# Kernel optimization log

Measured on AMD Instinct MI355X. Metric: run time of the kernel, lower is better.

Reference implementation:

```python
import jax, jax.numpy as jnp
import numpy as np

B, L, IN_DIM, OUT_DIM = 65536, 9, 128, 64


def setup_inputs() -> dict:
    key = jax.random.key(0)
    ks = jax.random.split(key, 9)
    s1 = 1.0 / np.sqrt(2 * IN_DIM)
    s2 = 1.0 / np.sqrt(IN_DIM)
    return {
        "value": jax.random.normal(ks[0], (B, L, IN_DIM), dtype=jnp.float32),
        "key": jax.random.normal(ks[1], (B, IN_DIM), dtype=jnp.float32),
        "seq_len": jax.random.randint(ks[2], (B,), 0, 8, dtype=jnp.int64),
        "maxlen": 9,
        # get_w: Linear(2*in_dim, in_dim) -> ReLU -> Linear(in_dim, 1)
        "w1": jax.random.uniform(ks[3], (IN_DIM, 2 * IN_DIM), jnp.float32, -s1, s1),
        "b1": jax.random.uniform(ks[4], (IN_DIM,), jnp.float32, -s1, s1),
        "w2": jax.random.uniform(ks[5], (1, IN_DIM), jnp.float32, -s2, s2),
        "b2": jax.random.uniform(ks[6], (1,), jnp.float32, -s2, s2),
        # fc: Linear(in_dim, out_dim) -> ReLU
        "fcw": jax.random.uniform(ks[7], (OUT_DIM, IN_DIM), jnp.float32, -s2, s2),
        "fcb": jax.random.uniform(ks[8], (OUT_DIM,), jnp.float32, -s2, s2),
    }


def reference(value, key, seq_len, maxlen, w1, b1, w2, b2, fcw, fcb):
    # value: [B, L, D]; key: [B, D]; L == maxlen
    Lv = value.shape[1]
    key_rep = jnp.broadcast_to(key[:, None, :], value.shape)          # [B, L, D]
    cat = jnp.concatenate([key_rep, value], axis=-1)                  # [B, L, 2D]
    h = jax.nn.relu(jnp.einsum("bld,hd->blh", cat, w1) + b1)          # [B, L, D]
    weight = (jnp.einsum("blh,oh->blo", h, w2) + b2)[..., 0]          # [B, L]
    # sequence_mask(seq_len + 1, maxlen): position t valid iff t+1 <= seq_len+1
    pos = jnp.arange(1, Lv + 1)                                       # [L]
    mask = pos[None, :] <= (seq_len + 1)[:, None]                     # [B, L] bool
    weight = jnp.where(mask, weight, -jnp.inf)
    attn = jax.nn.softmax(weight, axis=-1)                            # [B, L]
    out = jnp.einsum("bld,bl->bd", value, attn)                       # [B, D]
    out = jax.nn.relu(out @ fcw.T + fcb)                              # [B, out_dim]
    return out
```

## Files before the change

### kernel.cpp

```cpp
#include <hip/hip_runtime.h>
#include <hip/hip_bf16.h>

typedef __attribute__((ext_vector_type(8))) short short8;
typedef __attribute__((ext_vector_type(4))) float f32x4;

#define NW 8
#define BPW 16
#define BPB (NW * BPW)

static __device__ __forceinline__ unsigned pk_bf16(float a, float b) {
    unsigned d;
    asm("v_cvt_pk_bf16_f32 %0, %1, %2" : "=v"(d) : "v"(a), "v"(b));
    return d;
}

static __device__ __forceinline__ unsigned rne16(float x) {
    unsigned u = __float_as_uint(x);
    return (u + 0x7fffu + ((u >> 16) & 1u)) >> 16;
}
static __device__ __forceinline__ unsigned rne_bf16_pair(float x, float y) {
    return rne16(x) | (rne16(y) << 16);
}

static __device__ __forceinline__ short8 pack_frag(f32x4 a, f32x4 b) {
    union { unsigned u[4]; short8 s; } u;
    u.u[0] = pk_bf16(a.x, a.y);
    u.u[1] = pk_bf16(a.z, a.w);
    u.u[2] = pk_bf16(b.x, b.y);
    u.u[3] = pk_bf16(b.z, b.w);
    return u.s;
}

static __device__ __forceinline__ void stage_bfrags(const float* __restrict__ w,
                                                    int row_stride, int k_off, int nct,
                                                    short8* lds, int tid) {
    const int total = 4 * nct * 64;
    for (int idx = tid; idx < total; idx += NW * 64) {
        int lane = idx & 63;
        int ct = (idx >> 6) % nct;
        int kt = idx / (64 * nct);
        int n = ct * 16 + (lane & 15);
        int k = kt * 32 + (lane >> 4) * 8;
        const float* p = w + (size_t)n * row_stride + k_off + k;
        f32x4 a = *(const f32x4*)p;
        f32x4 b = *(const f32x4*)(p + 4);
        lds[idx] = pack_frag(a, b);
    }
}

static __device__ __forceinline__ void stage_bfrags_split(const float* __restrict__ w,
                                                          int row_stride, int nct,
                                                          short8* lds_hi, short8* lds_lo,
                                                          int tid) {
    const int total = 4 * nct * 64;
    for (int idx = tid; idx < total; idx += NW * 64) {
        int lane = idx & 63;
        int ct = (idx >> 6) % nct;
        int kt = idx / (64 * nct);
        int n = ct * 16 + (lane & 15);
        int k = kt * 32 + (lane >> 4) * 8;
        const float* p = w + (size_t)n * row_stride + k;
        f32x4 a = *(const f32x4*)p;
        f32x4 b = *(const f32x4*)(p + 4);
        float xs[8] = {a.x, a.y, a.z, a.w, b.x, b.y, b.z, b.w};
        union { unsigned u[4]; short8 s; } uh, ul;
#pragma unroll
        for (int q = 0; q < 4; ++q) {
            float x = xs[2 * q], y = xs[2 * q + 1];
            unsigned hx = rne16(x), hy = rne16(y);
            uh.u[q] = hx | (hy << 16);
            ul.u[q] = rne_bf16_pair(x - __uint_as_float(hx << 16),
                                    y - __uint_as_float(hy << 16));
        }
        lds_hi[idx] = uh.s;
        lds_lo[idx] = ul.s;
    }
}

__global__ __launch_bounds__(NW * 64, 2)
void mask_attn_fused(const float* __restrict__ value, const float* __restrict__ key,
                     const int* __restrict__ seq_len, const float* __restrict__ w1,
                     const float* __restrict__ b1, const float* __restrict__ w2,
                     const float* __restrict__ fcw, const float* __restrict__ fcb,
                     float* __restrict__ out, int B) {
    __shared__ short8 wlds[2048];

    const int tid = threadIdx.x;
    const int wave = tid >> 6;
    const int lane = tid & 63;
    const int g = lane >> 4;
    const int lo = lane & 15;

    const long long b0w = (long long)blockIdx.x * BPB + (long long)wave * BPW;
    long long vb = b0w + lo; if (vb > (long long)B - 1) vb = (long long)B - 1;

    stage_bfrags(w1, 2 * 128, 0, 8, wlds, tid);
    __syncthreads();

    unsigned hkp[8][2];
    {
        const float* kp = key + vb * 128 + g * 8;
        short8 af[4];
#pragma unroll
        for (int kt = 0; kt < 4; ++kt)
            af[kt] = pack_frag(*(const f32x4*)(kp + kt * 32), *(const f32x4*)(kp + kt * 32 + 4));
#pragma unroll
        for (int ct = 0; ct < 8; ++ct) {
            float bv = b1[ct * 16 + lo];
            f32x4 hk = (f32x4){bv, bv, bv, bv};
#pragma unroll
            for (int kt = 0; kt < 4; ++kt)
                hk = __builtin_amdgcn_mfma_f32_16x16x32_bf16(
                    af[kt], wlds[(kt * 8 + ct) * 64 + lane], hk, 0, 0, 0);
            hkp[ct][0] = rne_bf16_pair(hk.x, hk.y);
            hkp[ct][1] = rne_bf16_pair(hk.z, hk.w);
        }
    }
    __syncthreads();

    stage_bfrags(w1, 2 * 128, 128, 8, wlds, tid);
    __syncthreads();

    float w2v[8];
#pragma unroll
    for (int ct = 0; ct < 8; ++ct) w2v[ct] = w2[ct * 16 + lo];
    const int sq = seq_len[vb];

    float o[4][8];
#pragma unroll
    for (int kt = 0; kt < 4; ++kt)
#pragma unroll
        for (int j = 0; j < 8; ++j) o[kt][j] = 0.f;
    float s = 0.f, m = -3e38f;
    const float* ap = value + vb * (9 * 128) + g * 8;

#pragma unroll 1
    for (int l = 0; l < 9; ++l) {
        f32x4 va[8];
#pragma unroll
        for (int h = 0; h < 8; ++h)
            va[h] = *(const f32x4*)(ap + l * 128 + (h >> 1) * 32 + (h & 1) * 4);
        short8 af[4];
#pragma unroll
        for (int kt = 0; kt < 4; ++kt)
            af[kt] = pack_frag(va[2 * kt], va[2 * kt + 1]);

        float p0 = 0.f, p1 = 0.f, p2 = 0.f, p3 = 0.f;
#pragma unroll
        for (int ct = 0; ct < 8; ++ct) {
            f32x4 acc;
            acc.x = __uint_as_float(hkp[ct][0] << 16);
            acc.y = __uint_as_float(hkp[ct][0] & 0xffff0000u);
            acc.z = __uint_as_float(hkp[ct][1] << 16);
            acc.w = __uint_as_float(hkp[ct][1] & 0xffff0000u);
#pragma unroll
            for (int kt = 0; kt < 4; ++kt)
                acc = __builtin_amdgcn_mfma_f32_16x16x32_bf16(
                    af[kt], wlds[(kt * 8 + ct) * 64 + lane], acc, 0, 0, 0);
            p0 += fmaxf(acc.x, 0.f) * w2v[ct];
            p1 += fmaxf(acc.y, 0.f) * w2v[ct];
            p2 += fmaxf(acc.z, 0.f) * w2v[ct];
            p3 += fmaxf(acc.w, 0.f) * w2v[ct];
        }
#pragma unroll
        for (int mm = 1; mm <= 8; mm <<= 1) {
            p0 += __shfl_xor(p0, mm);
            p1 += __shfl_xor(p1, mm);
            p2 += __shfl_xor(p2, mm);
            p3 += __shfl_xor(p3, mm);
        }
        int sl = (lo >> 2) * 16;
        float t0 = __shfl(p0, sl), t1 = __shfl(p1, sl);
        float t2 = __shfl(p2, sl), t3 = __shfl(p3, sl);
        int r = lo & 3;
        float w = (r == 0) ? t0 : (r == 1) ? t1 : (r == 2) ? t2 : t3;

        bool valid = (l <= sq);
        float mn = valid ? fmaxf(m, w) : m;
        float c = __expf(m - mn);
        float e = valid ? __expf(w - mn) : 0.f;
        s = s * c + e;
        m = mn;
#pragma unroll
        for (int kt = 0; kt < 4; ++kt) {
            o[kt][0] = o[kt][0] * c + e * va[2 * kt].x;
            o[kt][1] = o[kt][1] * c + e * va[2 * kt].y;
            o[kt][2] = o[kt][2] * c + e * va[2 * kt].z;
            o[kt][3] = o[kt][3] * c + e * va[2 * kt].w;
            o[kt][4] = o[kt][4] * c + e * va[2 * kt + 1].x;
            o[kt][5] = o[kt][5] * c + e * va[2 * kt + 1].y;
            o[kt][6] = o[kt][6] * c + e * va[2 * kt + 1].z;
            o[kt][7] = o[kt][7] * c + e * va[2 * kt + 1].w;
        }
    }

    const float rs = 1.f / s;
    short8 afoh[4], afol[4];
#pragma unroll
    for (int kt = 0; kt < 4; ++kt) {
        union { unsigned u[4]; short8 v; } uh, ul;
#pragma unroll
        for (int p = 0; p < 4; ++p) {
            float x = o[kt][2 * p] * rs, y = o[kt][2 * p + 1] * rs;
            unsigned hx = rne16(x), hy = rne16(y);
            uh.u[p] = hx | (hy << 16);
            ul.u[p] = rne_bf16_pair(x - __uint_as_float(hx << 16),
                                    y - __uint_as_float(hy << 16));
        }
        afoh[kt] = uh.v;
        afol[kt] = ul.v;
    }

    __syncthreads();
    stage_bfrags_split(fcw, 128, 4, wlds, wlds + 1024, tid);
    __syncthreads();

    {
        f32x4 facc[4];
#pragma unroll
        for (int ct = 0; ct < 4; ++ct) {
            float fb = fcb[ct * 16 + lo];
            facc[ct] = (f32x4){fb, fb, fb, fb};
        }
#pragma unroll
        for (int kt = 0; kt < 4; ++kt)
#pragma unroll
            for (int ct = 0; ct < 4; ++ct) {
                short8 wh = wlds[(kt * 4 + ct) * 64 + lane];
                short8 wl = wlds[1024 + (kt * 4 + ct) * 64 + lane];
                facc[ct] = __builtin_amdgcn_mfma_f32_16x16x32_bf16(afoh[kt], wh, facc[ct], 0, 0, 0);
                facc[ct] = __builtin_amdgcn_mfma_f32_16x16x32_bf16(afol[kt], wh, facc[ct], 0, 0, 0);
                facc[ct] = __builtin_amdgcn_mfma_f32_16x16x32_bf16(afoh[kt], wl, facc[ct], 0, 0, 0);
            }
#pragma unroll
        for (int ct = 0; ct < 4; ++ct) {
            float v0 = fmaxf(facc[ct].x, 0.f), v1 = fmaxf(facc[ct].y, 0.f);
            float v2 = fmaxf(facc[ct].z, 0.f), v3 = fmaxf(facc[ct].w, 0.f);
            long long bo = b0w + g * 4;
            if (bo + 0 < B) out[(bo + 0) * 64 + ct * 16 + lo] = v0;
            if (bo + 1 < B) out[(bo + 1) * 64 + ct * 16 + lo] = v1;
            if (bo + 2 < B) out[(bo + 2) * 64 + ct * 16 + lo] = v2;
            if (bo + 3 < B) out[(bo + 3) * 64 + ct * 16 + lo] = v3;
        }
    }
}

extern "C" void kernel_launch(void* const* d_in, const int* in_sizes, int n_in,
                              void* d_out, int out_size, void* d_ws, size_t ws_size,
                              hipStream_t stream) {
    const float* value = (const float*)d_in[0];
    const float* key   = (const float*)d_in[1];
    const int*   seq   = (const int*)d_in[2];
    const float* w1    = (const float*)d_in[4];
    const float* b1    = (const float*)d_in[5];
    const float* w2    = (const float*)d_in[6];
    const float* fcw   = (const float*)d_in[8];
    const float* fcb   = (const float*)d_in[9];
    float* out = (float*)d_out;

    int B = in_sizes[1] / 128;
    int blocks = (B + BPB - 1) / BPB;
    mask_attn_fused<<<blocks, NW * 64, 0, stream>>>(value, key, seq, w1, b1, w2, fcw, fcb, out, B);
}
```

Baseline: 89.04 us.

## Prefetch next value row, move key-hidden and w2 to LDS, store values as bf16 hi/lo

Issues the loads for the next sequence position's value row before the MFMA work of the current one, so global memory latency overlaps compute. The per-lane key-hidden results and the w2 weights move from registers into shared memory to free VGPRs for the prefetch buffer. Each value row is kept as a bf16 hi/lo pair and rebuilt for the softmax accumulation, which adds ALU work and slightly changes numerics compared with the fp32 values. The extra LDS reads inside the inner loop and the larger shared-memory footprint could hurt occupancy at 2 blocks per CU.

```diff
diff --git a/kernel.cpp b/kernel.cpp
--- a/kernel.cpp
+++ b/kernel.cpp
@@ -84,6 +84,8 @@
                      const float* __restrict__ fcw, const float* __restrict__ fcb,
                      float* __restrict__ out, int B) {
     __shared__ short8 wlds[2048];
+    __shared__ uint2 hklds[NW * 8 * 64];
+    __shared__ float w2lds[128];
 
     const int tid = threadIdx.x;
     const int wave = tid >> 6;
@@ -94,16 +96,27 @@
     const long long b0w = (long long)blockIdx.x * BPB + (long long)wave * BPW;
     long long vb = b0w + lo; if (vb > (long long)B - 1) vb = (long long)B - 1;
 
+    const float* ap = value + vb * (9 * 128) + g * 8;
+    f32x4 raw[8];
+#pragma unroll
+    for (int h = 0; h < 8; ++h)
+        raw[h] = *(const f32x4*)(ap + (h >> 1) * 32 + (h & 1) * 4);
+    f32x4 kv[8];
+    const float* kp = key + vb * 128 + g * 8;
+#pragma unroll
+    for (int h = 0; h < 8; ++h)
+        kv[h] = *(const f32x4*)(kp + (h >> 1) * 32 + (h & 1) * 4);
+
+    if (tid < 128) w2lds[tid] = w2[tid];
+
     stage_bfrags(w1, 2 * 128, 0, 8, wlds, tid);
     __syncthreads();
 
-    unsigned hkp[8][2];
     {
-        const float* kp = key + vb * 128 + g * 8;
         short8 af[4];
 #pragma unroll
         for (int kt = 0; kt < 4; ++kt)
-            af[kt] = pack_frag(*(const f32x4*)(kp + kt * 32), *(const f32x4*)(kp + kt * 32 + 4));
+            af[kt] = pack_frag(kv[2 * kt], kv[2 * kt + 1]);
 #pragma unroll
         for (int ct = 0; ct < 8; ++ct) {
             float bv = b1[ct * 16 + lo];
@@ -112,8 +125,10 @@
             for (int kt = 0; kt < 4; ++kt)
                 hk = __builtin_amdgcn_mfma_f32_16x16x32_bf16(
                     af[kt], wlds[(kt * 8 + ct) * 64 + lane], hk, 0, 0, 0);
-            hkp[ct][0] = rne_bf16_pair(hk.x, hk.y);
-            hkp[ct][1] = rne_bf16_pair(hk.z, hk.w);
+            uint2 pk;
+            pk.x = rne_bf16_pair(hk.x, hk.y);
+            pk.y = rne_bf16_pair(hk.z, hk.w);
+            hklds[wave * 512 + ct * 64 + lane] = pk;
         }
     }
     __syncthreads();
@@ -121,10 +136,8 @@
     stage_bfrags(w1, 2 * 128, 128, 8, wlds, tid);
     __syncthreads();
 
-    float w2v[8];
-#pragma unroll
-    for (int ct = 0; ct < 8; ++ct) w2v[ct] = w2[ct * 16 + lo];
     const int sq = seq_len[vb];
+    const uint2* hkw = hklds + wave * 512;
 
     float o[4][8];
 #pragma unroll
@@ -132,35 +145,52 @@
 #pragma unroll
         for (int j = 0; j < 8; ++j) o[kt][j] = 0.f;
     float s = 0.f, m = -3e38f;
-    const float* ap = value + vb * (9 * 128) + g * 8;
 
 #pragma unroll 1
     for (int l = 0; l < 9; ++l) {
-        f32x4 va[8];
-#pragma unroll
-        for (int h = 0; h < 8; ++h)
-            va[h] = *(const f32x4*)(ap + l * 128 + (h >> 1) * 32 + (h & 1) * 4);
-        short8 af[4];
-#pragma unroll
-        for (int kt = 0; kt < 4; ++kt)
-            af[kt] = pack_frag(va[2 * kt], va[2 * kt + 1]);
+        short8 af[4], alo[4];
+#pragma unroll
+        for (int kt = 0; kt < 4; ++kt) {
+            f32x4 a = raw[2 * kt], b = raw[2 * kt + 1];
+            af[kt] = pack_frag(a, b);
+            float xs[8] = {a.x, a.y, a.z, a.w, b.x, b.y, b.z, b.w};
+            union { unsigned u[4]; short8 s; } ul;
+#pragma unroll
+            for (int q = 0; q < 4; ++q) {
+                float x = xs[2 * q], y = xs[2 * q + 1];
+                float hxf = __uint_as_float(__float_as_uint(x) & 0xffff0000u);
+                float hyf = __uint_as_float(__float_as_uint(y) & 0xffff0000u);
+                unsigned hx = rne16(x), hy = rne16(y);
+                (void)hxf; (void)hyf;
+                ul.u[q] = pk_bf16(x - __uint_as_float(hx << 16),
+                                  y - __uint_as_float(hy << 16));
+            }
+            alo[kt] = ul.s;
+        }
+        if (l + 1 < 9) {
+#pragma unroll
+            for (int h = 0; h < 8; ++h)
+                raw[h] = *(const f32x4*)(ap + (l + 1) * 128 + (h >> 1) * 32 + (h & 1) * 4);
+        }
 
         float p0 = 0.f, p1 = 0.f, p2 = 0.f, p3 = 0.f;
 #pragma unroll
         for (int ct = 0; ct < 8; ++ct) {
+            uint2 hkv = hkw[ct * 64 + lane];
             f32x4 acc;
-            acc.x = __uint_as_float(hkp[ct][0] << 16);
-            acc.y = __uint_as_float(hkp[ct][0] & 0xffff0000u);
-            acc.z = __uint_as_float(hkp[ct][1] << 16);
-            acc.w = __uint_as_float(hkp[ct][1] & 0xffff0000u);
+            acc.x = __uint_as_float(hkv.x << 16);
+            acc.y = __uint_as_float(hkv.x & 0xffff0000u);
+            acc.z = __uint_as_float(hkv.y << 16);
+            acc.w = __uint_as_float(hkv.y & 0xffff0000u);
 #pragma unroll
             for (int kt = 0; kt < 4; ++kt)
                 acc = __builtin_amdgcn_mfma_f32_16x16x32_bf16(
                     af[kt], wlds[(kt * 8 + ct) * 64 + lane], acc, 0, 0, 0);
-            p0 += fmaxf(acc.x, 0.f) * w2v[ct];
-            p1 += fmaxf(acc.y, 0.f) * w2v[ct];
-            p2 += fmaxf(acc.z, 0.f) * w2v[ct];
-            p3 += fmaxf(acc.w, 0.f) * w2v[ct];
+            float wv = w2lds[ct * 16 + lo];
+            p0 += fmaxf(acc.x, 0.f) * wv;
+            p1 += fmaxf(acc.y, 0.f) * wv;
+            p2 += fmaxf(acc.z, 0.f) * wv;
+            p3 += fmaxf(acc.w, 0.f) * wv;
         }
 #pragma unroll
         for (int mm = 1; mm <= 8; mm <<= 1) {
@@ -183,14 +213,18 @@
         m = mn;
 #pragma unroll
         for (int kt = 0; kt < 4; ++kt) {
-            o[kt][0] = o[kt][0] * c + e * va[2 * kt].x;
-            o[kt][1] = o[kt][1] * c + e * va[2 * kt].y;
-            o[kt][2] = o[kt][2] * c + e * va[2 * kt].z;
-            o[kt][3] = o[kt][3] * c + e * va[2 * kt].w;
-            o[kt][4] = o[kt][4] * c + e * va[2 * kt + 1].x;
-            o[kt][5] = o[kt][5] * c + e * va[2 * kt + 1].y;
-            o[kt][6] = o[kt][6] * c + e * va[2 * kt + 1].z;
-            o[kt][7] = o[kt][7] * c + e * va[2 * kt + 1].w;
+            union { short8 v; unsigned u[4]; } uh, ul;
+            uh.v = af[kt];
+            ul.v = alo[kt];
+#pragma unroll
+            for (int q = 0; q < 4; ++q) {
+                float h0 = __uint_as_float(uh.u[q] << 16);
+                float h1 = __uint_as_float(uh.u[q] & 0xffff0000u);
+                float l0 = __uint_as_float(ul.u[q] << 16);
+                float l1 = __uint_as_float(ul.u[q] & 0xffff0000u);
+                o[kt][2 * q]     = o[kt][2 * q] * c + e * (h0 + l0);
+                o[kt][2 * q + 1] = o[kt][2 * q + 1] * c + e * (h1 + l1);
+            }
         }
     }
 
```

Result: no change. 90.04 us (+1.1%).
